# Optimization experiments

Measured on AMD Instinct MI355X. Metric: run time of the kernel, lower is better.

## Reference

```python
import jax, jax.numpy as jnp
import numpy as np

KDIM = 128
NHEADS = 8
CAUSAL = True


def setup_inputs() -> dict:
    key = jax.random.key(0)
    ks = jax.random.split(key, 9)
    t, b = 1024, 8
    hk = KDIM * NHEADS
    s = 1.0 / np.sqrt(KDIM)
    return {
        "x":  jax.random.normal(ks[0], (t, b, KDIM), dtype=jnp.float32),
        "Wk": jax.random.uniform(ks[1], (hk, KDIM), jnp.float32, -s, s),
        "bk": jax.random.uniform(ks[2], (hk,), jnp.float32, -s, s),
        "Wq": jax.random.uniform(ks[3], (hk, KDIM), jnp.float32, -s, s),
        "bq": jax.random.uniform(ks[4], (hk,), jnp.float32, -s, s),
        "Wv": jax.random.uniform(ks[5], (hk, KDIM), jnp.float32, -s, s),
        "bv": jax.random.uniform(ks[6], (hk,), jnp.float32, -s, s),
        "Wo": jax.random.uniform(ks[7], (KDIM, hk), jnp.float32, -1.0/np.sqrt(hk), 1.0/np.sqrt(hk)),
        "bo": jax.random.uniform(ks[8], (KDIM,), jnp.float32, -1.0/np.sqrt(hk), 1.0/np.sqrt(hk)),
    }


def reference(x, Wk, bk, Wq, bq, Wv, bv, Wo, bo):
    t, b, _ = x.shape
    h, d = NHEADS, KDIM
    xb = jnp.transpose(x, (1, 0, 2))  # (b, t, d)

    def proj(W, bias):
        # (b, t, h*d) -> (b, h, t, d)
        y = xb @ W.T + bias
        return jnp.transpose(y.reshape(b, t, h, d), (0, 2, 1, 3))

    k_ = proj(Wk, bk)
    q_ = proj(Wq, bq)
    v_ = proj(Wv, bv)

    # NOTE: original computes bmm(key, query^T): rows indexed by KEY position.
    raw = jnp.einsum("bhik,bhjk->bhij", k_, q_) / jnp.sqrt(jnp.float32(d))
    if CAUSAL:
        # mask entries with col > row (upper triangle, offset 1)
        iidx = jnp.arange(t)[:, None]
        jidx = jnp.arange(t)[None, :]
        raw = jnp.where(jidx > iidx, -jnp.inf, raw)
    # softmax over the QUERY axis (dim=2 of the (bh,t,t) view == last axis here)
    att = jax.nn.softmax(raw, axis=-1)
    out = jnp.einsum("bhij,bhjd->bhid", att, v_)  # (b, h, t, d)
    out = jnp.transpose(out, (2, 0, 1, 3)).reshape(t, b, h * d)
    return out @ Wo.T + bo
```

## Files before the change

### kernel.cpp

```cpp
#include <hip/hip_runtime.h>
#include <hip/hip_bf16.h>

typedef __bf16 bf16_t;
typedef __bf16 bf16x2_t __attribute__((ext_vector_type(2)));
typedef __bf16 bf16x4_t __attribute__((ext_vector_type(4)));
typedef __bf16 bf16x8 __attribute__((ext_vector_type(8)));
typedef float f32x4 __attribute__((ext_vector_type(4)));
typedef float f32x16 __attribute__((ext_vector_type(16)));
typedef unsigned int u32x2 __attribute__((ext_vector_type(2)));

#define T_SEQ 1024
#define BATCH 8
#define NH 8
#define DH 128
#define HKDIM 1024

static __device__ __forceinline__ f32x4 mfma16(bf16x8 a, bf16x8 b, f32x4 c) {
    return __builtin_amdgcn_mfma_f32_16x16x32_bf16(a, b, c, 0, 0, 0);
}
static __device__ __forceinline__ f32x16 mfma32(bf16x8 a, bf16x8 b, f32x16 c) {
    return __builtin_amdgcn_mfma_f32_32x32x16_bf16(a, b, c, 0, 0, 0);
}

static __device__ __forceinline__ unsigned pk2(float a, float b) {
    bf16x2_t t;
    t[0] = (bf16_t)a;
    t[1] = (bf16_t)b;
    union { bf16x2_t v; unsigned u; } c;
    c.v = t;
    return c.u;
}

static __device__ __forceinline__ void plswap(unsigned& a, unsigned& b) {
    u32x2 r = __builtin_amdgcn_permlane32_swap(a, b, false, false);
    a = r[0];
    b = r[1];
}

static __device__ __forceinline__ float swap_partner(float x) {
    u32x2 r = __builtin_amdgcn_permlane32_swap(__float_as_uint(x),
                                               __float_as_uint(x), false, false);
    return __uint_as_float((threadIdx.x & 32) ? r[0] : r[1]);
}

__global__ __launch_bounds__(256) void convert_kernel(
        const float* __restrict__ x,
        const float* __restrict__ Wk, const float* __restrict__ Wq,
        const float* __restrict__ Wv, const float* __restrict__ Wo,
        bf16_t* __restrict__ xb, bf16_t* __restrict__ w3,
        bf16_t* __restrict__ wo) {
    const int n1 = T_SEQ * BATCH * DH;
    const int n2 = n1 + 3 * HKDIM * DH;
    const int n3 = n2 + DH * HKDIM;
    const int i = (blockIdx.x * 256 + threadIdx.x) * 4;
    if (i >= n3) return;
    const float* src;
    bf16_t* dst;
    if (i < n1) {
        int d = i & 127, t = (i >> 7) & 1023, b = i >> 17;
        src = x + (t * BATCH + b) * DH + d;
        dst = xb + i;
    } else if (i < n2) {
        int j = i - n1;
        int p = j >> 17;
        const float* W = (p == 0) ? Wk : (p == 1 ? Wq : Wv);
        src = W + (j & 131071);
        dst = w3 + j;
    } else {
        int j = i - n2;
        src = Wo + j;
        dst = wo + j;
    }
    f32x4 v = *(const f32x4*)src;
    bf16x4_t o;
    o[0] = (bf16_t)v[0]; o[1] = (bf16_t)v[1];
    o[2] = (bf16_t)v[2]; o[3] = (bf16_t)v[3];
    *(bf16x4_t*)dst = o;
}

__global__ __launch_bounds__(256) void proj_kernel(
        const bf16_t* __restrict__ xb, const bf16_t* __restrict__ w3,
        const float* __restrict__ bk, const float* __restrict__ bq,
        const float* __restrict__ bv,
        bf16_t* __restrict__ kbuf, bf16_t* __restrict__ qbuf,
        bf16_t* __restrict__ vtbuf) {
    const int lane = threadIdx.x & 63;
    const int wave = threadIdx.x >> 6;
    const int lr = lane & 15, lq = lane >> 4;
    const int rm_base = blockIdx.x * 128;
    const int cb0 = blockIdx.y * 64;
    const int p = cb0 >> 10;
    const int cw0 = cb0 & 1023;
    const int h = cw0 >> 7;
    const int dbase = cw0 & 127;
    const bool isV = (p == 2);

    __shared__ bf16_t sL[17408 / 2];

    bf16x8 aF[2][4];
#pragma unroll
    for (int rg = 0; rg < 2; ++rg) {
        const int row = rm_base + rg * 64 + wave * 16 + lr;
#pragma unroll
        for (int kc = 0; kc < 4; ++kc)
            aF[rg][kc] = *(const bf16x8*)(xb + (size_t)row * DH + kc * 32 + lq * 8);
    }

    const bf16_t* wbase = w3 + (size_t)(cb0 + lr) * DH + lq * 8;
    bf16x8 kcur[4], knxt[4];
#pragma unroll
    for (int kc = 0; kc < 4; ++kc)
        kcur[kc] = *(const bf16x8*)(wbase + kc * 32);

    const float* bias_kq = (p == 0) ? bk : bq;
    bf16_t* dst = (p == 0) ? kbuf : qbuf;

    bf16_t (*aL)[68] = (bf16_t(*)[68])sL;
    bf16_t (*vL)[136] = (bf16_t(*)[136])sL;

#pragma unroll
    for (int nc = 0; nc < 4; ++nc) {
        if (nc < 3) {
            const bf16_t* wn = wbase + (size_t)(nc + 1) * 16 * DH;
#pragma unroll
            for (int kc = 0; kc < 4; ++kc)
                knxt[kc] = *(const bf16x8*)(wn + kc * 32);
        }

        f32x4 acc[2] = {{0.f, 0.f, 0.f, 0.f}, {0.f, 0.f, 0.f, 0.f}};
        if (!isV) {
#pragma unroll
            for (int rg = 0; rg < 2; ++rg)
#pragma unroll
                for (int kc = 0; kc < 4; ++kc)
                    acc[rg] = mfma16(kcur[kc], aF[rg][kc], acc[rg]);

            const f32x4 b4 = *(const f32x4*)(bias_kq + cw0 + nc * 16 + lq * 4);
#pragma unroll
            for (int rg = 0; rg < 2; ++rg) {
                bf16x4_t o4;
#pragma unroll
                for (int r = 0; r < 4; ++r)
                    o4[r] = (bf16_t)(acc[rg][r] + b4[r]);
                *(bf16x4_t*)&aL[rg * 64 + wave * 16 + lr][nc * 16 + lq * 4] = o4;
            }
        } else {
#pragma unroll
            for (int rg = 0; rg < 2; ++rg)
#pragma unroll
                for (int kc = 0; kc < 4; ++kc)
                    acc[rg] = mfma16(aF[rg][kc], kcur[kc], acc[rg]);

            const float bias = bv[cw0 + nc * 16 + lr];
#pragma unroll
            for (int rg = 0; rg < 2; ++rg)
#pragma unroll
                for (int r = 0; r < 4; ++r)
                    vL[nc * 16 + lr][rg * 64 + wave * 16 + lq * 4 + r] =
                        (bf16_t)(acc[rg][r] + bias);
        }
        if (nc < 3) {
#pragma unroll
            for (int kc = 0; kc < 4; ++kc) kcur[kc] = knxt[kc];
        }
    }

    __syncthreads();
    const int tid = threadIdx.x;
    if (!isV) {
        const int tr = tid >> 3;
        const int d16 = tid & 7;
#pragma unroll
        for (int ps = 0; ps < 4; ++ps) {
            const int t_local = ps * 32 + tr;
            const int row = rm_base + t_local;
            const int bb = row >> 10, tt = row & 1023;
            bf16x8 v = *(const bf16x8*)&aL[t_local][d16 * 8];
            *(bf16x8*)(dst + ((size_t)(bb * NH + h) * T_SEQ + tt) * DH +
                       dbase + d16 * 8) = v;
        }
    } else {
        const int dl = tid >> 2;
        const int toff = (tid & 3) * 32;
        const int bb = blockIdx.x >> 3;
        const int t0 = (blockIdx.x & 7) * 128;
        const int dg = dbase + dl;
        bf16_t* dstv = vtbuf + ((size_t)(bb * NH + h) * DH + dg) * T_SEQ + t0 + toff;
#pragma unroll
        for (int i = 0; i < 4; ++i)
            *(bf16x8*)(dstv + i * 8) = *(const bf16x8*)&vL[dl][toff + i * 8];
    }
}

__global__ __launch_bounds__(256, 2) void attn_kernel(
        const bf16_t* __restrict__ kbuf, const bf16_t* __restrict__ qbuf,
        const bf16_t* __restrict__ vtb, bf16_t* __restrict__ obuf) {
    const int bx = blockIdx.x;
    const int T = (bx < 256) ? (7 - (bx >> 6)) : ((bx - 256) >> 6);
    const int bh = bx & 63;
    const int b = bh >> 3, h = bh & 7;
    const int wv = threadIdx.x >> 6;
    const int lane = threadIdx.x & 63;
    const int li = lane & 31;
    const int hi = lane >> 5;
    const int i0 = T * 128 + wv * 32;
    const int cmax = 4 * T + wv;
    const int nrounds = 2 * T + 2;

    const bf16_t* Qp = kbuf + (size_t)bh * T_SEQ * DH;
    const bf16_t* Kp = qbuf + (size_t)bh * T_SEQ * DH;
    const bf16_t* Vt = vtb + (size_t)bh * DH * T_SEQ;

    __shared__ bf16_t kL[64][136];
    __shared__ bf16_t vL[128][72];

    bf16x8 qf[8];
#pragma unroll
    for (int s = 0; s < 8; ++s)
        qf[s] = *(const bf16x8*)(Qp + (size_t)(i0 + li) * DH + s * 16 + hi * 8);

    f32x16 oacc[4];
#pragma unroll
    for (int c = 0; c < 4; ++c)
#pragma unroll
        for (int e = 0; e < 16; ++e) oacc[c][e] = 0.f;

    float m = 0.f, l = 0.f;
    const float C = 0.08838834764831845f * 1.4426950408889634f;

    const int tid = threadIdx.x;
    const int krow = tid >> 2;
    const int kcol = (tid & 3) * 32;
    const int vrow = tid >> 1;
    const int vcol = (tid & 1) * 32;
    const bf16_t* kgsrc = Kp + (size_t)krow * DH + kcol;
    const bf16_t* vgsrc = Vt + (size_t)vrow * T_SEQ + vcol;

    bf16x8 kr[4], vr[4];
#pragma unroll
    for (int i = 0; i < 4; ++i) {
        kr[i] = *(const bf16x8*)(kgsrc + i * 8);
        vr[i] = *(const bf16x8*)(vgsrc + i * 8);
    }

    for (int rd = 0; rd < nrounds; ++rd) {
        __syncthreads();
#pragma unroll
        for (int i = 0; i < 4; ++i) {
            *(bf16x8*)&kL[krow][kcol + i * 8] = kr[i];
            *(bf16x8*)&vL[vrow][vcol + i * 8] = vr[i];
        }
        if (rd + 1 < nrounds) {
            const bf16_t* kn = kgsrc + (size_t)(rd + 1) * 64 * DH;
            const bf16_t* vn = vgsrc + (size_t)(rd + 1) * 64;
#pragma unroll
            for (int i = 0; i < 4; ++i) {
                kr[i] = *(const bf16x8*)(kn + i * 8);
                vr[i] = *(const bf16x8*)(vn + i * 8);
            }
        }
        __syncthreads();

#pragma unroll
        for (int jj = 0; jj < 2; ++jj) {
            const int c32 = rd * 2 + jj;
            if (c32 > cmax) continue;

            bf16x8 ka[8];
#pragma unroll
            for (int s = 0; s < 8; ++s)
                ka[s] = *(const bf16x8*)&kL[jj * 32 + li][s * 16 + hi * 8];

            f32x16 sc;
#pragma unroll
            for (int e = 0; e < 16; ++e) sc[e] = 0.f;
            __builtin_amdgcn_s_setprio(1);
#pragma unroll
            for (int s = 0; s < 8; ++s) sc = mfma32(ka[s], qf[s], sc);
            __builtin_amdgcn_s_setprio(0);

            f32x16 sv;
#pragma unroll
            for (int e = 0; e < 16; ++e) sv[e] = sc[e] * C;
            if (c32 == cmax) {
#pragma unroll
                for (int r = 0; r < 16; ++r) {
                    const int jrow = (r & 3) + 8 * (r >> 2) + 4 * hi;
                    if (jrow > li) sv[r] = -1e30f;
                }
            }

            float pm = sv[0];
#pragma unroll
            for (int r = 1; r < 16; ++r) pm = fmaxf(pm, sv[r]);
            pm = fmaxf(pm, swap_partner(pm));

            if (!__all(pm <= m + 8.f)) {
                const float mn = fmaxf(m, pm);
                const float f = exp2f(m - mn);
                m = mn;
                l *= f;
#pragma unroll
                for (int cc = 0; cc < 4; ++cc)
#pragma unroll
                    for (int e = 0; e < 16; ++e) oacc[cc][e] *= f;
            }

            float ls = 0.f;
            unsigned Wp[8];
#pragma unroll
            for (int q = 0; q < 4; ++q) {
                const float p0 = exp2f(sv[4 * q + 0] - m);
                const float p1 = exp2f(sv[4 * q + 1] - m);
                const float p2 = exp2f(sv[4 * q + 2] - m);
                const float p3 = exp2f(sv[4 * q + 3] - m);
                ls += (p0 + p1) + (p2 + p3);
                Wp[2 * q] = pk2(p0, p1);
                Wp[2 * q + 1] = pk2(p2, p3);
            }
            l += ls;

            plswap(Wp[0], Wp[2]);
            plswap(Wp[1], Wp[3]);
            plswap(Wp[4], Wp[6]);
            plswap(Wp[5], Wp[7]);
            union { unsigned u[4]; bf16x8 v; } pb0, pb1;
            pb0.u[0] = Wp[0]; pb0.u[1] = Wp[1]; pb0.u[2] = Wp[2]; pb0.u[3] = Wp[3];
            pb1.u[0] = Wp[4]; pb1.u[1] = Wp[5]; pb1.u[2] = Wp[6]; pb1.u[3] = Wp[7];

            bf16x8 va[8];
#pragma unroll
            for (int n = 0; n < 4; ++n) {
                va[2 * n]     = *(const bf16x8*)&vL[li + 32 * n][jj * 32 + hi * 8];
                va[2 * n + 1] = *(const bf16x8*)&vL[li + 32 * n][jj * 32 + hi * 8 + 16];
            }
            __builtin_amdgcn_s_setprio(1);
            oacc[0] = mfma32(va[0], pb0.v, oacc[0]);
            oacc[0] = mfma32(va[1], pb1.v, oacc[0]);
            oacc[1] = mfma32(va[2], pb0.v, oacc[1]);
            oacc[1] = mfma32(va[3], pb1.v, oacc[1]);
            oacc[2] = mfma32(va[4], pb0.v, oacc[2]);
            oacc[2] = mfma32(va[5], pb1.v, oacc[2]);
            oacc[3] = mfma32(va[6], pb0.v, oacc[3]);
            oacc[3] = mfma32(va[7], pb1.v, oacc[3]);
            __builtin_amdgcn_s_setprio(0);
        }
    }

    const float lfull = l + swap_partner(l);
    const float inv = 1.f / lfull;
    bf16_t* orow = obuf + ((size_t)b * T_SEQ + i0 + li) * HKDIM + h * DH;
#pragma unroll
    for (int c = 0; c < 4; ++c)
#pragma unroll
        for (int q = 0; q < 4; ++q) {
            bf16x4_t o4;
#pragma unroll
            for (int rr = 0; rr < 4; ++rr)
                o4[rr] = (bf16_t)(oacc[c][4 * q + rr] * inv);
            *(bf16x4_t*)(orow + c * 32 + q * 8 + 4 * hi) = o4;
        }
}

__global__ __launch_bounds__(256) void outproj_kernel(
        const bf16_t* __restrict__ obuf, const bf16_t* __restrict__ wo,
        const float* __restrict__ bo, float* __restrict__ out) {
    const int lane = threadIdx.x & 63, wave = threadIdx.x >> 6;
    const int lr = lane & 15, lq = lane >> 4;
    const int rm0 = blockIdx.x * 16;
    __shared__ float red[4][8][256];

    f32x4 acc[8];
#pragma unroll
    for (int g = 0; g < 8; ++g) acc[g] = {0.f, 0.f, 0.f, 0.f};
#pragma unroll 2
    for (int k8 = 0; k8 < 8; ++k8) {
        const int kc = wave * 8 + k8;
        bf16x8 aF = *(const bf16x8*)(obuf + (size_t)(rm0 + lr) * HKDIM + kc * 32 + lq * 8);
#pragma unroll
        for (int g = 0; g < 8; ++g) {
            bf16x8 bF = *(const bf16x8*)(wo + (size_t)(g * 16 + lr) * HKDIM + kc * 32 + lq * 8);
            acc[g] = mfma16(aF, bF, acc[g]);
        }
    }
#pragma unroll
    for (int g = 0; g < 8; ++g)
        *(f32x4*)&red[wave][g][lane * 4] = acc[g];
    __syncthreads();
#pragma unroll
    for (int gi = 0; gi < 2; ++gi) {
        const int g = wave * 2 + gi;
        f32x4 s = *(const f32x4*)&red[0][g][lane * 4];
#pragma unroll
        for (int w = 1; w < 4; ++w) {
            f32x4 t = *(const f32x4*)&red[w][g][lane * 4];
            s[0] += t[0]; s[1] += t[1]; s[2] += t[2]; s[3] += t[3];
        }
        const int col = g * 16 + lr;
        const float bias = bo[col];
#pragma unroll
        for (int r = 0; r < 4; ++r) {
            const int row = rm0 + lq * 4 + r;
            const int bb = row >> 10, tt = row & 1023;
            out[((size_t)tt * BATCH + bb) * DH + col] = s[r] + bias;
        }
    }
}

extern "C" void kernel_launch(void* const* d_in, const int* in_sizes, int n_in,
                              void* d_out, int out_size, void* d_ws, size_t ws_size,
                              hipStream_t stream) {
    const float* x  = (const float*)d_in[0];
    const float* Wk = (const float*)d_in[1];
    const float* bk = (const float*)d_in[2];
    const float* Wq = (const float*)d_in[3];
    const float* bq = (const float*)d_in[4];
    const float* Wv = (const float*)d_in[5];
    const float* bv = (const float*)d_in[6];
    const float* Wo = (const float*)d_in[7];
    const float* bo = (const float*)d_in[8];
    float* out = (float*)d_out;

    char* ws = (char*)d_ws;
    size_t off = 0;
    bf16_t* xb  = (bf16_t*)(ws + off); off += (size_t)BATCH * T_SEQ * DH * 2;
    bf16_t* w3  = (bf16_t*)(ws + off); off += (size_t)3 * HKDIM * DH * 2;
    bf16_t* wo  = (bf16_t*)(ws + off); off += (size_t)DH * HKDIM * 2;
    bf16_t* kb  = (bf16_t*)(ws + off); off += (size_t)BATCH * NH * T_SEQ * DH * 2;
    bf16_t* qb  = (bf16_t*)(ws + off); off += (size_t)BATCH * NH * T_SEQ * DH * 2;
    bf16_t* vtb = (bf16_t*)(ws + off); off += (size_t)BATCH * NH * T_SEQ * DH * 2;
    bf16_t* ob  = (bf16_t*)(ws + off); off += (size_t)BATCH * T_SEQ * HKDIM * 2;

    convert_kernel<<<1536, 256, 0, stream>>>(x, Wk, Wq, Wv, Wo, xb, w3, wo);
    proj_kernel<<<dim3(64, 48), 256, 0, stream>>>(xb, w3, bk, bq, bv, kb, qb, vtb);
    attn_kernel<<<512, 256, 0, stream>>>(kb, qb, vtb, ob);
    outproj_kernel<<<512, 256, 0, stream>>>(ob, wo, bo, out);
}
```

Measured before the change: 107.2 us.

## Widen projection tiles to full head and stage attention output via LDS

New measurement: 100.2 us. -6.5%, faster.

```diff
diff --git a/kernel.cpp b/kernel.cpp
--- a/kernel.cpp
+++ b/kernel.cpp
@@ -88,14 +88,13 @@
     const int wave = threadIdx.x >> 6;
     const int lr = lane & 15, lq = lane >> 4;
     const int rm_base = blockIdx.x * 128;
-    const int cb0 = blockIdx.y * 64;
-    const int p = cb0 >> 10;
-    const int cw0 = cb0 & 1023;
-    const int h = cw0 >> 7;
-    const int dbase = cw0 & 127;
+    const int p = blockIdx.y >> 3;
+    const int h = blockIdx.y & 7;
+    const int cb0 = p * 1024 + h * 128;
+    const int cw0 = h * 128;
     const bool isV = (p == 2);
 
-    __shared__ bf16_t sL[17408 / 2];
+    __shared__ bf16_t sL[128][136];
 
     bf16x8 aF[2][4];
 #pragma unroll
@@ -115,12 +114,9 @@
     const float* bias_kq = (p == 0) ? bk : bq;
     bf16_t* dst = (p == 0) ? kbuf : qbuf;
 
-    bf16_t (*aL)[68] = (bf16_t(*)[68])sL;
-    bf16_t (*vL)[136] = (bf16_t(*)[136])sL;
-
-#pragma unroll
-    for (int nc = 0; nc < 4; ++nc) {
-        if (nc < 3) {
+#pragma unroll
+    for (int nc = 0; nc < 8; ++nc) {
+        if (nc < 7) {
             const bf16_t* wn = wbase + (size_t)(nc + 1) * 16 * DH;
 #pragma unroll
             for (int kc = 0; kc < 4; ++kc)
@@ -142,7 +138,7 @@
 #pragma unroll
                 for (int r = 0; r < 4; ++r)
                     o4[r] = (bf16_t)(acc[rg][r] + b4[r]);
-                *(bf16x4_t*)&aL[rg * 64 + wave * 16 + lr][nc * 16 + lq * 4] = o4;
+                *(bf16x4_t*)&sL[rg * 64 + wave * 16 + lr][nc * 16 + lq * 4] = o4;
             }
         } else {
 #pragma unroll
@@ -156,10 +152,10 @@
             for (int rg = 0; rg < 2; ++rg)
 #pragma unroll
                 for (int r = 0; r < 4; ++r)
-                    vL[nc * 16 + lr][rg * 64 + wave * 16 + lq * 4 + r] =
+                    sL[nc * 16 + lr][rg * 64 + wave * 16 + lq * 4 + r] =
                         (bf16_t)(acc[rg][r] + bias);
         }
-        if (nc < 3) {
+        if (nc < 7) {
 #pragma unroll
             for (int kc = 0; kc < 4; ++kc) kcur[kc] = knxt[kc];
         }
@@ -168,27 +164,28 @@
     __syncthreads();
     const int tid = threadIdx.x;
     if (!isV) {
-        const int tr = tid >> 3;
-        const int d16 = tid & 7;
-#pragma unroll
-        for (int ps = 0; ps < 4; ++ps) {
-            const int t_local = ps * 32 + tr;
+        const int tr = tid >> 4;
+        const int ck = tid & 15;
+#pragma unroll
+        for (int ps = 0; ps < 8; ++ps) {
+            const int t_local = ps * 16 + tr;
             const int row = rm_base + t_local;
             const int bb = row >> 10, tt = row & 1023;
-            bf16x8 v = *(const bf16x8*)&aL[t_local][d16 * 8];
-            *(bf16x8*)(dst + ((size_t)(bb * NH + h) * T_SEQ + tt) * DH +
-                       dbase + d16 * 8) = v;
+            bf16x8 v = *(const bf16x8*)&sL[t_local][ck * 8];
+            *(bf16x8*)(dst + ((size_t)(bb * NH + h) * T_SEQ + tt) * DH + ck * 8) = v;
         }
     } else {
-        const int dl = tid >> 2;
-        const int toff = (tid & 3) * 32;
+        const int dr = tid >> 4;
+        const int ck = tid & 15;
         const int bb = blockIdx.x >> 3;
         const int t0 = (blockIdx.x & 7) * 128;
-        const int dg = dbase + dl;
-        bf16_t* dstv = vtbuf + ((size_t)(bb * NH + h) * DH + dg) * T_SEQ + t0 + toff;
-#pragma unroll
-        for (int i = 0; i < 4; ++i)
-            *(bf16x8*)(dstv + i * 8) = *(const bf16x8*)&vL[dl][toff + i * 8];
+#pragma unroll
+        for (int ps = 0; ps < 8; ++ps) {
+            const int d = ps * 16 + dr;
+            bf16x8 v = *(const bf16x8*)&sL[d][ck * 8];
+            *(bf16x8*)(vtbuf + ((size_t)(bb * NH + h) * DH + d) * T_SEQ +
+                       t0 + ck * 8) = v;
+        }
     }
 }
 
@@ -349,7 +346,10 @@
 
     const float lfull = l + swap_partner(l);
     const float inv = 1.f / lfull;
-    bf16_t* orow = obuf + ((size_t)b * T_SEQ + i0 + li) * HKDIM + h * DH;
+    __syncthreads();
+    bf16_t (*oL)[136] = (bf16_t(*)[136])kL;
+    bf16_t* base = (wv < 2) ? &kL[0][0] : &vL[0][0];
+    const int rloc = (wv & 1) * 32 + li;
 #pragma unroll
     for (int c = 0; c < 4; ++c)
 #pragma unroll
@@ -358,8 +358,22 @@
 #pragma unroll
             for (int rr = 0; rr < 4; ++rr)
                 o4[rr] = (bf16_t)(oacc[c][4 * q + rr] * inv);
-            *(bf16x4_t*)(orow + c * 32 + q * 8 + 4 * hi) = o4;
-        }
+            *(bf16x4_t*)(base + (size_t)rloc * 136 + c * 32 + q * 8 + 4 * hi) = o4;
+        }
+    __syncthreads();
+    {
+        const int tr = tid >> 4;
+        const int ck = tid & 15;
+#pragma unroll
+        for (int ps = 0; ps < 8; ++ps) {
+            const int rl = ps * 16 + tr;
+            const bf16_t* src = ((rl & 64) ? &vL[0][0] : &kL[0][0]) +
+                                (size_t)(rl & 63) * 136 + ck * 8;
+            bf16x8 v = *(const bf16x8*)src;
+            const int row = T * 128 + rl;
+            *(bf16x8*)(obuf + ((size_t)b * T_SEQ + row) * HKDIM + h * DH + ck * 8) = v;
+        }
+    }
 }
 
 __global__ __launch_bounds__(256) void outproj_kernel(
@@ -432,7 +446,7 @@
     bf16_t* ob  = (bf16_t*)(ws + off); off += (size_t)BATCH * T_SEQ * HKDIM * 2;
 
     convert_kernel<<<1536, 256, 0, stream>>>(x, Wk, Wq, Wv, Wo, xb, w3, wo);
-    proj_kernel<<<dim3(64, 48), 256, 0, stream>>>(xb, w3, bk, bq, bv, kb, qb, vtb);
+    proj_kernel<<<dim3(64, 24), 256, 0, stream>>>(xb, w3, bk, bq, bv, kb, qb, vtb);
     attn_kernel<<<512, 256, 0, stream>>>(kb, qb, vtb, ob);
     outproj_kernel<<<512, 256, 0, stream>>>(ob, wo, bo, out);
 }
```
